# Performance work log

Hardware: AMD Instinct MI355X
Metric: run time of the kernel (lower is better)

## Reference

```python
import jax, jax.numpy as jnp
import numpy as np

B, L, D, H = 8, 1024, 1024, 16
DK = D // H  # 64
LN_EPS = 1e-5
L2_EPS = 1e-12


def _l2norm(x):
    # torch F.normalize(dim=-1): x / max(||x||_2, eps)
    n = jnp.sqrt(jnp.sum(x * x, axis=-1, keepdims=True))
    return x / jnp.maximum(n, L2_EPS)


def _layernorm(x, gamma, beta):
    mu = jnp.mean(x, axis=-1, keepdims=True)
    var = jnp.mean((x - mu) ** 2, axis=-1, keepdims=True)
    return (x - mu) * jax.lax.rsqrt(var + LN_EPS) * gamma + beta


def setup_inputs() -> dict:
    key = jax.random.key(0)
    ks = jax.random.split(key, 12)
    s = 0.02
    inp = {
        "Q": jax.random.normal(ks[0], (B, L, D), jnp.float32),
        "ctx": jax.random.normal(ks[1], (B, L, D), jnp.float32),
        "attn_mask": jnp.triu(jnp.ones((L, L), bool), 1),  # True = masked (causal)
        # weights stored [in, out] (= torch weight.T) so y = x @ W + b
        "W_q": jax.random.normal(ks[2], (D, D), jnp.float32) * s,
        "b_q": jnp.zeros((D,), jnp.float32),
        "W_k": jax.random.normal(ks[3], (D, D), jnp.float32) * s,
        "b_k": jnp.zeros((D,), jnp.float32),
        "W_v": jax.random.normal(ks[4], (D, D), jnp.float32) * s,
        "b_v": jnp.zeros((D,), jnp.float32),
        "bilinear": jax.random.normal(ks[5], (DK, DK), jnp.float32),
        "ln_gamma": jnp.ones((DK,), jnp.float32),
        "ln_beta": jnp.zeros((DK,), jnp.float32),
        "scale": jnp.asarray(DK ** -0.5, jnp.float32),
        "bias_scale": jnp.asarray(0.1, jnp.float32),
        "W_o": jax.random.normal(ks[6], (D, D), jnp.float32) * s,
        "b_o": jnp.zeros((D,), jnp.float32),
    }
    return inp


def reference(Q, ctx, attn_mask, W_q, b_q, W_k, b_k, W_v, b_v, bilinear,
              ln_gamma, ln_beta, scale, bias_scale, W_o, b_o):
    def split_heads(x):  # [B,L,D] -> [B,H,L,DK]
        return x.reshape(B, L, H, DK).transpose(0, 2, 1, 3)

    q = split_heads(Q @ W_q + b_q)
    k = split_heads(Q @ W_k + b_k)  # self-attention: K = V = Q
    v = split_heads(Q @ W_v + b_v)

    scores = jnp.einsum("bhqd,bhkd->bhqk", q, k) * scale  # [B,H,L,L]
    scores = jnp.where(attn_mask, -jnp.inf, scores)
    attn = jax.nn.softmax(scores, axis=-1)

    # post-softmax bilinear bias: LayerNorm -> bilinear matmul -> L2-normalize
    c = _layernorm(split_heads(ctx), ln_gamma, ln_beta)  # [B,H,L,DK]
    bias = jnp.einsum("bhqe,bhke->bhqk", c @ bilinear, c)  # [B,H,L,L]
    attn = attn + _l2norm(bias) * bias_scale
    attn = _l2norm(attn)

    out = jnp.einsum("bhqk,bhkd->bhqd", attn, v)  # [B,H,L,DK]
    out = out.transpose(0, 2, 1, 3).reshape(B, L, D)
    out = out @ W_o + b_o
    return out
```

## Files before the change

### kernel.cpp

```cpp
#include <hip/hip_runtime.h>


typedef __bf16 bf16;
typedef __bf16 bf16x8 __attribute__((ext_vector_type(8)));
typedef __bf16 bf16x4 __attribute__((ext_vector_type(4)));
typedef float  f32x4  __attribute__((ext_vector_type(4)));

#define DEV static __device__ __forceinline__

DEV f32x4 mfma16(bf16x8 a, bf16x8 b, f32x4 c) {
  return __builtin_amdgcn_mfma_f32_16x16x32_bf16(a, b, c, 0, 0, 0);
}

DEV void async16(void* lds, const void* g) {
  auto* d = reinterpret_cast<__attribute__((address_space(3))) unsigned int*>(
      (unsigned long long)lds);
  auto* s = reinterpret_cast<const __attribute__((address_space(1))) unsigned int*>(
      (unsigned long long)g);
  __builtin_amdgcn_global_load_lds(s, d, 16, 0, 0);
}


__global__ __launch_bounds__(256) void k_cvt(const float* __restrict__ in,
                                             bf16* __restrict__ out, int n4) {
  int i = blockIdx.x * 256 + threadIdx.x;
  if (i >= n4) return;
  f32x4 v = ((const f32x4*)in)[i];
  bf16x4 o = {(bf16)v.x, (bf16)v.y, (bf16)v.z, (bf16)v.w};
  ((bf16x4*)out)[i] = o;
}

__global__ __launch_bounds__(256) void k_transpose_w(const float* __restrict__ in,
                                                     bf16* __restrict__ out) {
  __shared__ float t[64][65];
  const int k0 = blockIdx.x * 64, n0 = blockIdx.y * 64;
  for (int e = threadIdx.x; e < 4096; e += 256) {
    int r = e >> 6, c = e & 63;
    t[r][c] = in[(size_t)(k0 + r) * 1024 + n0 + c];
  }
  __syncthreads();
  for (int e = threadIdx.x; e < 4096; e += 256) {
    int r = e >> 6, c = e & 63;
    out[(size_t)(n0 + r) * 1024 + k0 + c] = (bf16)t[c][r];
  }
}

__global__ __launch_bounds__(256) void k_transpose_v(const bf16* __restrict__ in,
                                                     bf16* __restrict__ out) {
  __shared__ bf16 t[64][65];
  const int bh = blockIdx.y, k0 = blockIdx.x * 64;
  const bf16* src = in + (size_t)bh * 65536;
  bf16* dst = out + (size_t)bh * 65536;
  for (int e = threadIdx.x; e < 4096; e += 256) {
    int r = e >> 6, c = e & 63;
    t[r][c] = src[(size_t)(k0 + r) * 64 + c];
  }
  __syncthreads();
  for (int e = threadIdx.x; e < 4096; e += 256) {
    int r = e >> 6, c = e & 63;
    dst[(size_t)r * 1024 + k0 + c] = t[c][r];
  }
}

__global__ __launch_bounds__(256) void k_ln_bilinear(
    const float* __restrict__ ctx, const float* __restrict__ bil,
    const float* __restrict__ gam, const float* __restrict__ bet,
    bf16* __restrict__ c_out, bf16* __restrict__ cb_out) {
  __shared__ float cs[4][64];
  const int w = threadIdx.x >> 6, lane = threadIdx.x & 63;
  const int wid = blockIdx.x * 4 + w;
  const int h = wid & 15, bl = wid >> 4;
  const float x = ctx[(size_t)bl * 1024 + h * 64 + lane];
  float s1 = x, s2 = x * x;
#pragma unroll
  for (int m = 32; m >= 1; m >>= 1) {
    s1 += __shfl_xor(s1, m);
    s2 += __shfl_xor(s2, m);
  }
  const float mu = s1 * 0.015625f;
  const float var = s2 * 0.015625f - mu * mu;
  const float cv = (x - mu) * rsqrtf(var + 1e-5f) * gam[lane] + bet[lane];
  const size_t o = ((size_t)((bl >> 10) * 16 + h) * 1024 + (bl & 1023)) * 64 + lane;
  c_out[o] = (bf16)cv;
  cs[w][lane] = cv;
  __syncthreads();
  float acc = 0.f;
#pragma unroll 8
  for (int e = 0; e < 64; ++e) acc += cs[w][e] * bil[e * 64 + lane];
  cb_out[o] = (bf16)acc;
}


struct GemmPtrs {
  const bf16* Bt[3];
  bf16* ob[3];
  const float* bias[3];
};

__global__ __launch_bounds__(256) void k_gemm(const bf16* __restrict__ A,
                                              GemmPtrs p,
                                              float* __restrict__ outf,
                                              int mode) {
  __shared__ __align__(16) bf16 lds[2][2][4096];
  const int tid = threadIdx.x;
  const int bm = blockIdx.x, bn = blockIdx.y, z = blockIdx.z;
  const int w = tid >> 6, lane = tid & 63, g = lane >> 4, x = lane & 15;
  const int wr = w >> 1, wc = w & 1;
  const bf16* Bt = p.Bt[z];
  const float* bias = p.bias[z];
  bf16* ob = p.ob[z];

  f32x4 acc[4][4];
#pragma unroll
  for (int mt = 0; mt < 4; ++mt)
#pragma unroll
    for (int nt = 0; nt < 4; ++nt) acc[mt][nt] = f32x4{0.f, 0.f, 0.f, 0.f};

  const bf16* Ab = A + (size_t)bm * 128 * 1024;
  const bf16* Bb = Bt + (size_t)bn * 128 * 1024;

  auto stage = [&](int buf, int t) {
#pragma unroll
    for (int i = 0; i < 2; ++i) {
      int ch = i * 256 + tid;
      int r = ch >> 2, s = ch & 3;
      int sg = (s ^ ((r >> 1) & 3)) * 8;
      async16(&lds[buf][0][ch * 8], Ab + (size_t)r * 1024 + t * 32 + sg);
      async16(&lds[buf][1][ch * 8], Bb + (size_t)r * 1024 + t * 32 + sg);
    }
  };

  stage(0, 0);
  const int sa = (g ^ ((x >> 1) & 3)) * 8;
  for (int kt = 0; kt < 32; ++kt) {
    __syncthreads();
    if (kt + 1 < 32) stage((kt + 1) & 1, kt + 1);
    const bf16* la = lds[kt & 1][0];
    const bf16* lb = lds[kt & 1][1];
    bf16x8 af[4], bfr[4];
#pragma unroll
    for (int mt = 0; mt < 4; ++mt)
      af[mt] = *(const bf16x8*)(la + (wr * 64 + mt * 16 + x) * 32 + sa);
#pragma unroll
    for (int nt = 0; nt < 4; ++nt)
      bfr[nt] = *(const bf16x8*)(lb + (wc * 64 + nt * 16 + x) * 32 + sa);
#pragma unroll
    for (int mt = 0; mt < 4; ++mt)
#pragma unroll
      for (int nt = 0; nt < 4; ++nt)
        acc[mt][nt] = mfma16(af[mt], bfr[nt], acc[mt][nt]);
  }

  const int ibase = bm * 128 + wr * 64;
  const int jbase = bn * 128 + wc * 64;
  float bias4[4];
#pragma unroll
  for (int nt = 0; nt < 4; ++nt) bias4[nt] = bias[jbase + nt * 16 + x];

  if (mode < 3) {
#pragma unroll
    for (int mt = 0; mt < 4; ++mt)
#pragma unroll
      for (int nt = 0; nt < 4; ++nt) {
        const int jj = jbase + nt * 16 + x;
        const int hh = jj >> 6, dk = jj & 63;
#pragma unroll
        for (int j = 0; j < 4; ++j) {
          const int i = ibase + mt * 16 + 4 * g + j;
          const int bb = i >> 10, l = i & 1023;
          ob[(((size_t)bb * 16 + hh) * 1024 + l) * 64 + dk] =
              (bf16)(acc[mt][nt][j] + bias4[nt]);
        }
      }
  } else {
#pragma unroll
    for (int mt = 0; mt < 4; ++mt)
#pragma unroll
      for (int nt = 0; nt < 4; ++nt) {
        const int jj = jbase + nt * 16 + x;
#pragma unroll
        for (int j = 0; j < 4; ++j) {
          const int i = ibase + mt * 16 + 4 * g + j;
          outf[(size_t)i * 1024 + jj] = acc[mt][nt][j] + bias4[nt];
        }
      }
  }
}

__global__ __launch_bounds__(256, 4) void k_attn(
    const bf16* __restrict__ qg, const bf16* __restrict__ kg,
    const bf16* __restrict__ vTg, const bf16* __restrict__ cg,
    const bf16* __restrict__ cbg, bf16* __restrict__ ao,
    const float* __restrict__ scale_p, const float* __restrict__ bsp) {
  __shared__ __align__(16) bf16 kl[2][2048];
  __shared__ __align__(16) bf16 cl[2][2048];
  __shared__ __align__(16) bf16 vl[2][64][40];
  __shared__ __align__(16) bf16 pe[4][640];
  __shared__ __align__(16) bf16 pb[4][640];

  const float scl = scale_p[0];
  const float bsc = bsp[0];
  const int tid = threadIdx.x, w = tid >> 6, lane = tid & 63;
  const int g = lane >> 4, x = lane & 15;
  const int id = blockIdx.x;
  const int xcd = id & 7, sid = id >> 3;
  const int bh = xcd * 16 + (sid >> 4);
  const int qt = sid & 15;
  const int qrow0 = qt * 64 + w * 16;

  const bf16* qrow = qg + ((size_t)bh * 1024 + qrow0 + x) * 64;
  const bf16* cbrow = cbg + ((size_t)bh * 1024 + qrow0 + x) * 64;
  const bf16x8 qf0 = *(const bf16x8*)(qrow + 8 * g);
  const bf16x8 qf1 = *(const bf16x8*)(qrow + 32 + 8 * g);
  const bf16x8 cbf0 = *(const bf16x8*)(cbrow + 8 * g);
  const bf16x8 cbf1 = *(const bf16x8*)(cbrow + 32 + 8 * g);

  f32x4 acc1[4], acc2[4];
#pragma unroll
  for (int i = 0; i < 4; ++i) {
    acc1[i] = f32x4{0.f, 0.f, 0.f, 0.f};
    acc2[i] = f32x4{0.f, 0.f, 0.f, 0.f};
  }
  float Zs = 0.f, E2 = 0.f, Cc = 0.f, B2 = 0.f;

  const bf16* kbh = kg + (size_t)bh * 65536;
  const bf16* cbh = cg + (size_t)bh * 65536;
  const bf16* vbh = vTg + (size_t)bh * 65536;
  const int nK = 2 * qt + 2;

  auto stageKC = [&](int buf, int t) {
    const int r = tid >> 3, s = tid & 7;
    const int sg = (s ^ (r & 7)) * 8;
    if (t < nK)
      async16(&kl[buf][tid * 8], kbh + (size_t)(t * 32 + r) * 64 + sg);
    async16(&cl[buf][tid * 8], cbh + (size_t)(t * 32 + r) * 64 + sg);
  };
  bf16x8 vreg;
  auto loadV = [&](int t) {
    const int r = tid >> 2, s = tid & 3;
    vreg = *(const bf16x8*)(vbh + (size_t)r * 1024 + t * 32 + s * 8);
  };
  auto writeV = [&](int buf) {
    const int r = tid >> 2, s = tid & 3;
    *(bf16x8*)&vl[buf][r][(s ^ (r & 3)) * 8] = vreg;
  };

  stageKC(0, 0);
  loadV(0);
  writeV(0);
  for (int t = 0; t < 32; ++t) {
    __syncthreads();
    if (t + 1 < 32) {
      stageKC((t + 1) & 1, t + 1);
      loadV(t + 1);
    }
    const bf16* klb = kl[t & 1];
    const bf16* clb = cl[t & 1];
    const int tileK = t * 32;
    const bool hv = tileK <= qrow0 + 15;
    float sv[8], bv[8];
#pragma unroll
    for (int sub = 0; sub < 2; ++sub) {
      const int rloc = sub * 16 + x;
      const int so0 = (g ^ (rloc & 7)) * 8;
      const int so1 = ((4 + g) ^ (rloc & 7)) * 8;
      const bf16* cr = clb + rloc * 64;
      f32x4 bacc = f32x4{0.f, 0.f, 0.f, 0.f};
      bacc = mfma16(*(const bf16x8*)(cr + so0), cbf0, bacc);
      bacc = mfma16(*(const bf16x8*)(cr + so1), cbf1, bacc);
      const int k16 = tileK + sub * 16;
      const bool av = k16 <= qrow0 + 15;
      const bool full = (k16 + 15) <= qrow0;
      f32x4 sacc = f32x4{0.f, 0.f, 0.f, 0.f};
      if (av) {
        const bf16* kr = klb + rloc * 64;
        sacc = mfma16(*(const bf16x8*)(kr + so0), qf0, sacc);
        sacc = mfma16(*(const bf16x8*)(kr + so1), qf1, sacc);
      }
      const int q = qrow0 + x;
#pragma unroll
      for (int j = 0; j < 4; ++j) {
        bv[sub * 4 + j] = bacc[j];
        B2 += bacc[j] * bacc[j];
        const int kk = k16 + 4 * g + j;
        sv[sub * 4 + j] =
            full ? sacc[j] * scl
                 : ((av && kk <= q) ? sacc[j] * scl : -1e30f);
      }
    }
    if (hv) {
      float ev[8];
#pragma unroll
      for (int jj = 0; jj < 8; ++jj) {
        const float e = __expf(sv[jj]);
        ev[jj] = e;
        Zs += e; E2 += e * e; Cc += e * bv[jj];
      }
      bf16x4 e0 = {(bf16)ev[0], (bf16)ev[1], (bf16)ev[2], (bf16)ev[3]};
      bf16x4 e1 = {(bf16)ev[4], (bf16)ev[5], (bf16)ev[6], (bf16)ev[7]};
      *(bf16x4*)&pe[w][x * 40 + 4 * g] = e0;
      *(bf16x4*)&pe[w][x * 40 + 16 + 4 * g] = e1;
    }
    bf16x4 b0 = {(bf16)bv[0], (bf16)bv[1], (bf16)bv[2], (bf16)bv[3]};
    bf16x4 b1 = {(bf16)bv[4], (bf16)bv[5], (bf16)bv[6], (bf16)bv[7]};
    *(bf16x4*)&pb[w][x * 40 + 4 * g] = b0;
    *(bf16x4*)&pb[w][x * 40 + 16 + 4 * g] = b1;
    const bf16x8 pbf = *(const bf16x8*)&pb[w][x * 40 + 8 * g];
#pragma unroll
    for (int nt = 0; nt < 4; ++nt) {
      const int dr = nt * 16 + x;
      const bf16x8 vf = *(const bf16x8*)&vl[t & 1][dr][(g ^ (dr & 3)) * 8];
      acc2[nt] = mfma16(pbf, vf, acc2[nt]);
    }
    if (hv) {
      const bf16x8 pef = *(const bf16x8*)&pe[w][x * 40 + 8 * g];
#pragma unroll
      for (int nt = 0; nt < 4; ++nt) {
        const int dr = nt * 16 + x;
        const bf16x8 vf = *(const bf16x8*)&vl[t & 1][dr][(g ^ (dr & 3)) * 8];
        acc1[nt] = mfma16(pef, vf, acc1[nt]);
      }
    }
    if (t + 1 < 32) writeV((t + 1) & 1);
  }

  Zs += __shfl_xor(Zs, 16); Zs += __shfl_xor(Zs, 32);
  E2 += __shfl_xor(E2, 16); E2 += __shfl_xor(E2, 32);
  Cc += __shfl_xor(Cc, 16); Cc += __shfl_xor(Cc, 32);
  B2 += __shfl_xor(B2, 16); B2 += __shfl_xor(B2, 32);
  const float bnorm = fmaxf(sqrtf(B2), 1e-12f);
  const float invZ = 1.0f / Zs;
  const float n2 = E2 * invZ * invZ + 2.0f * bsc * Cc * invZ / bnorm +
                   bsc * bsc * B2 / (bnorm * bnorm);
  const float inv_an = 1.0f / fmaxf(sqrtf(n2), 1e-12f);
  const float cA = invZ * inv_an;
  const float cB = bsc / bnorm * inv_an;
  const int b_ = bh >> 4, h_ = bh & 15;
#pragma unroll
  for (int j = 0; j < 4; ++j) {
    const int src = (lane & 48) | (4 * g + j);
    const float cAj = __shfl(cA, src);
    const float cBj = __shfl(cB, src);
    const int qr = qrow0 + 4 * g + j;
#pragma unroll
    for (int nt = 0; nt < 4; ++nt) {
      const float o = cAj * acc1[nt][j] + cBj * acc2[nt][j];
      ao[(size_t)(b_ * 1024 + qr) * 1024 + h_ * 64 + nt * 16 + x] = (bf16)o;
    }
  }
}


extern "C" void kernel_launch(void* const* d_in, const int* in_sizes, int n_in,
                              void* d_out, int out_size, void* d_ws,
                              size_t ws_size, hipStream_t stream) {
  const float* Q   = (const float*)d_in[0];
  const float* ctx = (const float*)d_in[1];
  const float* Wq  = (const float*)d_in[3];
  const float* bq  = (const float*)d_in[4];
  const float* Wk  = (const float*)d_in[5];
  const float* bk  = (const float*)d_in[6];
  const float* Wv  = (const float*)d_in[7];
  const float* bvp = (const float*)d_in[8];
  const float* bil = (const float*)d_in[9];
  const float* gam = (const float*)d_in[10];
  const float* bet = (const float*)d_in[11];
  const float* scl = (const float*)d_in[12];
  const float* bsc = (const float*)d_in[13];
  const float* Wo  = (const float*)d_in[14];
  const float* bo  = (const float*)d_in[15];
  float* out = (float*)d_out;
  char* ws = (char*)d_ws;
  const size_t MB = 1ull << 20;

  bf16* Qb  = (bf16*)(ws + 0);
  bf16* Wtq = (bf16*)(ws + 16 * MB);
  bf16* Wtk = (bf16*)(ws + 18 * MB);
  bf16* Wtv = (bf16*)(ws + 20 * MB);
  bf16* Wto = (bf16*)(ws + 22 * MB);
  bf16* qb  = (bf16*)(ws + 24 * MB);
  bf16* kb  = (bf16*)(ws + 40 * MB);
  bf16* vb  = (bf16*)(ws + 56 * MB);
  bf16* vT  = (bf16*)(ws + 72 * MB);
  bf16* cN  = (bf16*)(ws + 88 * MB);
  bf16* cbN = (bf16*)(ws + 104 * MB);
  bf16* ao  = Qb;

  k_cvt<<<8192, 256, 0, stream>>>(Q, Qb, 2097152);
  k_transpose_w<<<dim3(16, 16), 256, 0, stream>>>(Wq, Wtq);
  k_transpose_w<<<dim3(16, 16), 256, 0, stream>>>(Wk, Wtk);
  k_transpose_w<<<dim3(16, 16), 256, 0, stream>>>(Wv, Wtv);
  k_transpose_w<<<dim3(16, 16), 256, 0, stream>>>(Wo, Wto);
  k_ln_bilinear<<<32768, 256, 0, stream>>>(ctx, bil, gam, bet, cN, cbN);

  GemmPtrs p1{{Wtq, Wtk, Wtv}, {qb, kb, vb}, {bq, bk, bvp}};
  k_gemm<<<dim3(64, 8, 3), 256, 0, stream>>>(Qb, p1, nullptr, 0);

  k_transpose_v<<<dim3(16, 128), 256, 0, stream>>>(vb, vT);
  k_attn<<<2048, 256, 0, stream>>>(qb, kb, vT, cN, cbN, ao, scl, bsc);

  GemmPtrs p2{{Wto, Wto, Wto}, {nullptr, nullptr, nullptr}, {bo, bo, bo}};
  k_gemm<<<dim3(64, 8, 1), 256, 0, stream>>>(ao, p2, out, 3);

  (void)in_sizes; (void)n_in; (void)out_size; (void)ws_size;
}
```

Before: 474.4 us.

## Fuse V transpose into QKV GEMM epilogue and vectorize bilinear matvec

The V projection GEMM now writes its output directly in transposed [bh][dk][l] layout with 4-wide bf16 stores, so the separate V transpose kernel and its extra round trip through memory are removed. The bilinear matrix is pre-transposed once so the LayerNorm/bilinear kernel can read each lane's row as contiguous float4 loads instead of strided scalar loads. The padding of the V tile in LDS in the attention kernel is also shrunk from 40 to 36 columns, which changes the LDS bank pattern and may add conflicts.

```diff
diff --git a/kernel.cpp b/kernel.cpp
--- a/kernel.cpp
+++ b/kernel.cpp
@@ -45,25 +45,17 @@
   }
 }
 
-__global__ __launch_bounds__(256) void k_transpose_v(const bf16* __restrict__ in,
-                                                     bf16* __restrict__ out) {
-  __shared__ bf16 t[64][65];
-  const int bh = blockIdx.y, k0 = blockIdx.x * 64;
-  const bf16* src = in + (size_t)bh * 65536;
-  bf16* dst = out + (size_t)bh * 65536;
-  for (int e = threadIdx.x; e < 4096; e += 256) {
-    int r = e >> 6, c = e & 63;
-    t[r][c] = src[(size_t)(k0 + r) * 64 + c];
-  }
+__global__ __launch_bounds__(256) void k_transpose_bil(
+    const float* __restrict__ in, float* __restrict__ out) {
+  __shared__ float t[64][65];
+  for (int e = threadIdx.x; e < 4096; e += 256) t[e >> 6][e & 63] = in[e];
   __syncthreads();
-  for (int e = threadIdx.x; e < 4096; e += 256) {
-    int r = e >> 6, c = e & 63;
-    dst[(size_t)r * 1024 + k0 + c] = t[c][r];
-  }
+  for (int e = threadIdx.x; e < 4096; e += 256)
+    out[e] = t[e & 63][e >> 6];
 }
 
 __global__ __launch_bounds__(256) void k_ln_bilinear(
-    const float* __restrict__ ctx, const float* __restrict__ bil,
+    const float* __restrict__ ctx, const float* __restrict__ bilT,
     const float* __restrict__ gam, const float* __restrict__ bet,
     bf16* __restrict__ c_out, bf16* __restrict__ cb_out) {
   __shared__ float cs[4][64];
@@ -84,9 +76,14 @@
   c_out[o] = (bf16)cv;
   cs[w][lane] = cv;
   __syncthreads();
+  const f32x4* brow = (const f32x4*)(bilT + (size_t)lane * 64);
   float acc = 0.f;
-#pragma unroll 8
-  for (int e = 0; e < 64; ++e) acc += cs[w][e] * bil[e * 64 + lane];
+#pragma unroll
+  for (int e4 = 0; e4 < 16; ++e4) {
+    const f32x4 b4 = brow[e4];
+    const f32x4 c4 = *(const f32x4*)&cs[w][e4 * 4];
+    acc += c4.x * b4.x + c4.y * b4.y + c4.z * b4.z + c4.w * b4.w;
+  }
   cb_out[o] = (bf16)acc;
 }
 
@@ -158,20 +155,37 @@
   for (int nt = 0; nt < 4; ++nt) bias4[nt] = bias[jbase + nt * 16 + x];
 
   if (mode < 3) {
-#pragma unroll
-    for (int mt = 0; mt < 4; ++mt)
-#pragma unroll
-      for (int nt = 0; nt < 4; ++nt) {
-        const int jj = jbase + nt * 16 + x;
-        const int hh = jj >> 6, dk = jj & 63;
-#pragma unroll
-        for (int j = 0; j < 4; ++j) {
-          const int i = ibase + mt * 16 + 4 * g + j;
-          const int bb = i >> 10, l = i & 1023;
-          ob[(((size_t)bb * 16 + hh) * 1024 + l) * 64 + dk] =
-              (bf16)(acc[mt][nt][j] + bias4[nt]);
+    if (z == 2) {
+#pragma unroll
+      for (int mt = 0; mt < 4; ++mt)
+#pragma unroll
+        for (int nt = 0; nt < 4; ++nt) {
+          const int jj = jbase + nt * 16 + x;
+          const int hh = jj >> 6, dk = jj & 63;
+          const int i0 = ibase + mt * 16 + 4 * g;
+          const int bb = i0 >> 10, l0 = i0 & 1023;
+          bf16x4 v4 = {(bf16)(acc[mt][nt][0] + bias4[nt]),
+                       (bf16)(acc[mt][nt][1] + bias4[nt]),
+                       (bf16)(acc[mt][nt][2] + bias4[nt]),
+                       (bf16)(acc[mt][nt][3] + bias4[nt])};
+          *(bf16x4*)&ob[((size_t)(bb * 16 + hh) * 64 + dk) * 1024 + l0] = v4;
         }
-      }
+    } else {
+#pragma unroll
+      for (int mt = 0; mt < 4; ++mt)
+#pragma unroll
+        for (int nt = 0; nt < 4; ++nt) {
+          const int jj = jbase + nt * 16 + x;
+          const int hh = jj >> 6, dk = jj & 63;
+#pragma unroll
+          for (int j = 0; j < 4; ++j) {
+            const int i = ibase + mt * 16 + 4 * g + j;
+            const int bb = i >> 10, l = i & 1023;
+            ob[(((size_t)bb * 16 + hh) * 1024 + l) * 64 + dk] =
+                (bf16)(acc[mt][nt][j] + bias4[nt]);
+          }
+        }
+    }
   } else {
 #pragma unroll
     for (int mt = 0; mt < 4; ++mt)
@@ -194,7 +208,7 @@
     const float* __restrict__ scale_p, const float* __restrict__ bsp) {
   __shared__ __align__(16) bf16 kl[2][2048];
   __shared__ __align__(16) bf16 cl[2][2048];
-  __shared__ __align__(16) bf16 vl[2][64][40];
+  __shared__ __align__(16) bf16 vl[2][64][36];
   __shared__ __align__(16) bf16 pe[4][640];
   __shared__ __align__(16) bf16 pb[4][640];
 
@@ -380,10 +394,10 @@
   bf16* Wto = (bf16*)(ws + 22 * MB);
   bf16* qb  = (bf16*)(ws + 24 * MB);
   bf16* kb  = (bf16*)(ws + 40 * MB);
-  bf16* vb  = (bf16*)(ws + 56 * MB);
   bf16* vT  = (bf16*)(ws + 72 * MB);
   bf16* cN  = (bf16*)(ws + 88 * MB);
   bf16* cbN = (bf16*)(ws + 104 * MB);
+  float* bilT = (float*)(ws + 120 * MB);
   bf16* ao  = Qb;
 
   k_cvt<<<8192, 256, 0, stream>>>(Q, Qb, 2097152);
@@ -391,12 +405,12 @@
   k_transpose_w<<<dim3(16, 16), 256, 0, stream>>>(Wk, Wtk);
   k_transpose_w<<<dim3(16, 16), 256, 0, stream>>>(Wv, Wtv);
   k_transpose_w<<<dim3(16, 16), 256, 0, stream>>>(Wo, Wto);
-  k_ln_bilinear<<<32768, 256, 0, stream>>>(ctx, bil, gam, bet, cN, cbN);
-
-  GemmPtrs p1{{Wtq, Wtk, Wtv}, {qb, kb, vb}, {bq, bk, bvp}};
+  k_transpose_bil<<<1, 256, 0, stream>>>(bil, bilT);
+  k_ln_bilinear<<<32768, 256, 0, stream>>>(ctx, bilT, gam, bet, cN, cbN);
+
+  GemmPtrs p1{{Wtq, Wtk, Wtv}, {qb, kb, vT}, {bq, bk, bvp}};
   k_gemm<<<dim3(64, 8, 3), 256, 0, stream>>>(Qb, p1, nullptr, 0);
 
-  k_transpose_v<<<dim3(16, 128), 256, 0, stream>>>(vb, vT);
   k_attn<<<2048, 256, 0, stream>>>(qb, kb, vT, cN, cbN, ao, scl, bsc);
 
   GemmPtrs p2{{Wto, Wto, Wto}, {nullptr, nullptr, nullptr}, {bo, bo, bo}};
```

New measurement: 612.0 us. 1.29x slower.
